# Optimization experiments

Measured on AMD Instinct MI355X. Metric: run time of the kernel, lower is better.

The kernel has to match this reference:

```python
import jax, jax.numpy as jnp
import numpy as np

N_LEVELS = 128.0  # int8: [-128, 127]

def fake_quant(x):
    """Per-tensor int8 fixed-point fake quant (power-of-two scale), STE rounding."""
    maxabs = jnp.max(jnp.abs(x))
    # power-of-two scale covering maxabs, as in Brevitas *FixedPoint quantizers
    scale = jnp.exp2(jnp.ceil(jnp.log2(jnp.maximum(maxabs, 1e-10)))) / N_LEVELS
    scale = jax.lax.stop_gradient(scale)
    xs = x / scale
    q = jnp.clip(jnp.round(xs), -N_LEVELS, N_LEVELS - 1.0)
    q = xs + jax.lax.stop_gradient(q - xs)  # straight-through estimator
    return q * scale


def setup_inputs() -> dict:
    key = jax.random.key(0)
    k1, k2, k3, k4 = jax.random.split(key, 4)
    B, T, D, H = 512, 2048, 10, 20
    x = jax.random.normal(k1, (B, T, D), dtype=jnp.float32)
    h0 = jnp.zeros((B, H), dtype=jnp.float32)
    W_ih = jax.random.normal(k2, (H, D), dtype=jnp.float32) * 0.3
    W_hh = jax.random.normal(k3, (H, H), dtype=jnp.float32) * 0.2
    b = jax.random.normal(k4, (H,), dtype=jnp.float32) * 0.1
    return {"x": x, "h0": h0, "W_ih": W_ih, "W_hh": W_hh, "b": b}


def reference(x, h0, W_ih, W_hh, b):
    # io quant on input and initial state
    xq = fake_quant(x)
    h = fake_quant(h0)
    # weight / bias quant (per-tensor fixed point)
    Wi = fake_quant(W_ih)
    Wh = fake_quant(W_hh)
    bq = fake_quant(b)
    # precompute input-hidden contribution for all timesteps: [B,T,H]
    xW = jnp.einsum('btd,hd->bth', xq, Wi) + bq

    def step(h_prev, xw_t):
        acc = xw_t + h_prev @ Wh.T          # gate accumulation [B,H]
        acc = fake_quant(acc)               # gate_acc_quant
        h_new = jnp.tanh(acc)               # vanilla RNN nonlinearity
        out = fake_quant(h_new)             # io_quant on output/hidden
        return out, out

    xW_t = jnp.swapaxes(xW, 0, 1)           # [T,B,H]
    _, outs = jax.lax.scan(step, h, xW_t)   # outs: [T,B,H]
    return jnp.swapaxes(outs, 0, 1)         # batch_first output [B,T,H]
```

## Files before the change

kernel.cpp:

```cpp
#include <hip/hip_runtime.h>
#include <math.h>

#define BB 512
#define TT 2048
#define DD 10
#define HH 20
#define BH (BB*HH)

#define WS_AMAX     0
#define WS_PROD_XWI 4
#define WS_INV_SX   5
#define WS_S_H0     6
#define WS_INV_SH0  7
#define WS_S_WH     8
#define WS_BQ       16
#define WS_WIP      40
#define WS_WHP      104
#define WS_XW_OFF   4096

#define BAR() asm volatile("s_waitcnt lgkmcnt(0)\n\ts_barrier" ::: "memory")

__device__ __forceinline__ int dot4(int a, int b, int c) {
#if defined(__has_builtin)
#if __has_builtin(__builtin_amdgcn_sdot4)
    return __builtin_amdgcn_sdot4(a, b, c, false);
#define DOT4_DONE 1
#endif
#endif
#ifndef DOT4_DONE
    int r = c;
    r += ((a << 24) >> 24) * ((b << 24) >> 24);
    r += ((a << 16) >> 24) * ((b << 16) >> 24);
    r += ((a << 8) >> 24) * ((b << 8) >> 24);
    r += (a >> 24) * (b >> 24);
    return r;
#endif
}

__device__ __forceinline__ void p2s(float m, float* s, float* is) {
    m = fmaxf(m, 1e-10f);
    unsigned u = __float_as_uint(m);
    int k = (int)(u >> 23) - 127 + ((u & 0x7fffffu) ? 1 : 0);
    *s  = __uint_as_float((unsigned)(k + 120) << 23);
    *is = __uint_as_float((unsigned)(134 - k) << 23);
}

__device__ __forceinline__ int qlevel(float v, float inv) {
    return (int)fminf(fmaxf(rintf(v * inv), -128.f), 127.f);
}

__device__ __forceinline__ int pack4(int a, int b, int c, int d) {
    return (a & 255) | ((b & 255) << 8) | ((c & 255) << 16) | ((d & 255) << 24);
}

__global__ void k_amax(const float* __restrict__ x, int n4, unsigned* amax) {
    int g = blockIdx.x * blockDim.x + threadIdx.x;
    int stride = gridDim.x * blockDim.x;
    const float4* xv = (const float4*)x;
    float m = 0.f;
    for (int i = g; i < n4; i += stride) {
        float4 v = xv[i];
        m = fmaxf(m, fmaxf(fmaxf(fabsf(v.x), fabsf(v.y)), fmaxf(fabsf(v.z), fabsf(v.w))));
    }
#pragma unroll
    for (int off = 32; off; off >>= 1) m = fmaxf(m, __shfl_xor(m, off, 64));
    if ((threadIdx.x & 63) == 0) atomicMax(amax, __float_as_uint(m));
}

__device__ float bmaxabs(const float* p, int n, float* red, int tid) {
    float m = 0.f;
    for (int i = tid; i < n; i += 256) m = fmaxf(m, fabsf(p[i]));
    red[tid] = m; __syncthreads();
    for (int s = 128; s; s >>= 1) {
        if (tid < s) red[tid] = fmaxf(red[tid], red[tid + s]);
        __syncthreads();
    }
    m = red[0]; __syncthreads();
    return m;
}

__global__ void k_prep(const float* __restrict__ Wi, const float* __restrict__ Wh,
                       const float* __restrict__ bias, const float* __restrict__ h0,
                       float* wsf, int* wsi) {
    __shared__ float red[256];
    __shared__ float hdr[4];
    int tid = threadIdx.x;
    float mwi = bmaxabs(Wi, HH * DD, red, tid);
    float mwh = bmaxabs(Wh, HH * HH, red, tid);
    float mb  = bmaxabs(bias, HH, red, tid);
    float mh0 = bmaxabs(h0, BH, red, tid);
    if (tid == 0) {
        float mx = __uint_as_float(((unsigned*)wsf)[WS_AMAX]);
        float sx, isx, swi, iswi, swh, iswh, sb, isb, sh0, ish0;
        p2s(mx,  &sx,  &isx);
        p2s(mwi, &swi, &iswi);
        p2s(mwh, &swh, &iswh);
        p2s(mb,  &sb,  &isb);
        p2s(mh0, &sh0, &ish0);
        wsf[WS_PROD_XWI] = sx * swi;
        wsf[WS_INV_SX]   = isx;
        wsf[WS_S_H0]     = sh0;
        wsf[WS_INV_SH0]  = ish0;
        wsf[WS_S_WH]     = swh;
        hdr[0] = iswi; hdr[1] = iswh; hdr[2] = sb; hdr[3] = isb;
    }
    __syncthreads();
    if (tid < HH) {
        float iswi = hdr[0], iswh = hdr[1], sb = hdr[2], isb = hdr[3];
        int lv[20];
#pragma unroll
        for (int d = 0; d < DD; ++d) lv[d] = qlevel(Wi[tid * DD + d], iswi);
        lv[10] = 0; lv[11] = 0;
#pragma unroll
        for (int k = 0; k < 3; ++k)
            wsi[WS_WIP + tid * 3 + k] = pack4(lv[4*k], lv[4*k+1], lv[4*k+2], lv[4*k+3]);
#pragma unroll
        for (int k = 0; k < HH; ++k) lv[k] = qlevel(Wh[tid * HH + k], iswh);
#pragma unroll
        for (int k = 0; k < 5; ++k)
            wsi[WS_WHP + tid * 5 + k] = pack4(lv[4*k], lv[4*k+1], lv[4*k+2], lv[4*k+3]);
        wsf[WS_BQ + tid] = (float)qlevel(bias[tid], isb) * sb;
    }
}

__global__ __launch_bounds__(256) void k_xw(const float* __restrict__ x,
                                            const float* __restrict__ wsf,
                                            const int* __restrict__ wsi,
                                            float* __restrict__ xw) {
    int g = blockIdx.x * 256 + threadIdx.x;
    int b = g & (BB - 1);
    int t = g >> 9;
    float isx  = wsf[WS_INV_SX];
    float prod = wsf[WS_PROD_XWI];
    const float2* xp = (const float2*)(x + ((size_t)b * TT + t) * DD);
    float xv[10];
#pragma unroll
    for (int k = 0; k < 5; ++k) { float2 v = xp[k]; xv[2*k] = v.x; xv[2*k+1] = v.y; }
    int lv[12];
#pragma unroll
    for (int d = 0; d < DD; ++d) lv[d] = qlevel(xv[d], isx);
    lv[10] = 0; lv[11] = 0;
    int xpk[3];
#pragma unroll
    for (int k = 0; k < 3; ++k) xpk[k] = pack4(lv[4*k], lv[4*k+1], lv[4*k+2], lv[4*k+3]);
    float res[20];
#pragma unroll
    for (int j = 0; j < HH; ++j) {
        int ai = 0;
#pragma unroll
        for (int k = 0; k < 3; ++k) ai = dot4(xpk[k], wsi[WS_WIP + j * 3 + k], ai);
        res[j] = (float)ai * prod + wsf[WS_BQ + j];
    }
    float4* op = (float4*)(xw + (size_t)t * BH + b * HH);
#pragma unroll
    for (int k = 0; k < 5; ++k)
        op[k] = make_float4(res[4*k], res[4*k+1], res[4*k+2], res[4*k+3]);
}

__global__ __launch_bounds__(1024) void k_rnn(const float* __restrict__ h0,
                                              const float* __restrict__ wsf,
                                              const int* __restrict__ wsi,
                                              float* __restrict__ xw) {
    __shared__ float2 wred[16];
    __shared__ float4 bc;
    __shared__ int lut[256];
    const int tid = threadIdx.x;
    const int b = tid >> 1;
    const int jb = (tid & 1) * 10;
    const bool isLo = (tid & 1) == 0;
    const float s_wh = wsf[WS_S_WH];
    float sprod = wsf[WS_S_H0] * s_wh;

    int whp[50];
#pragma unroll
    for (int jj = 0; jj < 10; ++jj)
#pragma unroll
        for (int k = 0; k < 5; ++k)
            whp[jj * 5 + k] = wsi[WS_WHP + (jb + jj) * 5 + k];

    int hd[5];
    {
        float ish0 = wsf[WS_INV_SH0];
        const float2* hp = (const float2*)(h0 + b * HH + jb);
        int lv[10];
#pragma unroll
        for (int k = 0; k < 5; ++k) {
            float2 v = hp[k];
            lv[2*k]   = qlevel(v.x, ish0);
            lv[2*k+1] = qlevel(v.y, ish0);
        }
        int PA = pack4(lv[0], lv[1], lv[2], lv[3]);
        int PB = pack4(lv[4], lv[5], lv[6], lv[7]);
        int PC = (lv[8] & 255) | ((lv[9] & 255) << 8);
        int QA = __shfl_xor(PA, 1, 64);
        int QB = __shfl_xor(PB, 1, 64);
        int QC = __shfl_xor(PC, 1, 64);
        int XA = isLo ? PA : QA, XB = isLo ? PB : QB, XC = isLo ? PC : QC;
        int YA = isLo ? QA : PA, YB = isLo ? QB : PB, YC = isLo ? QC : PC;
        hd[0] = XA; hd[1] = XB;
        hd[2] = (XC & 0xFFFF) | (YA << 16);
        hd[3] = ((unsigned)YA >> 16) | (YB << 16);
        hd[4] = ((unsigned)YB >> 16) | (YC << 16);
    }
    float xwA[10];
    {
        const float2* p = (const float2*)(xw + b * HH + jb);
#pragma unroll
        for (int k = 0; k < 5; ++k) { float2 v = p[k]; xwA[2*k] = v.x; xwA[2*k+1] = v.y; }
    }

    for (int t = 0; t < TT; ++t) {
        float xwB[10];
        if (t + 1 < TT) {
            const float2* p = (const float2*)(xw + (size_t)(t + 1) * BH + b * HH + jb);
#pragma unroll
            for (int k = 0; k < 5; ++k) { float2 v = p[k]; xwB[2*k] = v.x; xwB[2*k+1] = v.y; }
        }
        float acc[10];
#pragma unroll
        for (int jj = 0; jj < 10; ++jj) {
            int ai = 0;
#pragma unroll
            for (int k = 0; k < 5; ++k) ai = dot4(hd[k], whp[jj * 5 + k], ai);
            acc[jj] = xwA[jj] + (float)ai * sprod;
        }
        float mx = acc[0], nmi = -acc[0];
#pragma unroll
        for (int jj = 1; jj < 10; ++jj) { mx = fmaxf(mx, acc[jj]); nmi = fmaxf(nmi, -acc[jj]); }
#pragma unroll
        for (int off = 32; off; off >>= 1) {
            mx  = fmaxf(mx,  __shfl_xor(mx,  off, 64));
            nmi = fmaxf(nmi, __shfl_xor(nmi, off, 64));
        }
        if ((tid & 63) == 0) wred[tid >> 6] = make_float2(mx, nmi);
        BAR();
        float isa, sh;
        float sprodN;
        if (tid < 256) {
            float2 p = wred[tid & 15];
            float ma = p.x, nm = p.y;
#pragma unroll
            for (int off = 8; off; off >>= 1) {
                ma = fmaxf(ma, __shfl_xor(ma, off, 64));
                nm = fmaxf(nm, __shfl_xor(nm, off, 64));
            }
            float sa;
            p2s(fmaxf(ma, nm), &sa, &isa);
            float lp = fminf(fmaxf(rintf(ma * isa), -128.f), 127.f);
            float ln = fminf(fmaxf(rintf(-nm * isa), -128.f), 127.f);
            float mlvl = fmaxf(fabsf(lp), fabsf(ln));
            float mh = tanhf(mlvl * sa);
            float ish;
            p2s(mh, &sh, &ish);
            sprodN = sh * s_wh;
            float tq = tanhf((float)(tid - 128) * sa);
            lut[tid] = (int)fminf(fmaxf(rintf(tq * ish), -128.f), 127.f);
            if (tid == 0) bc = make_float4(isa, sh, sprodN, 0.f);
        }
        BAR();
        if (tid >= 256) {
            float4 v = bc;
            isa = v.x; sh = v.y; sprod = v.z;
        } else {
            sprod = sprodN;
        }
        int ql[10];
#pragma unroll
        for (int jj = 0; jj < 10; ++jj) {
            int qi = (int)fminf(fmaxf(rintf(acc[jj] * isa), -128.f), 127.f);
            ql[jj] = lut[128 + qi];
        }
        {
            float2* op = (float2*)(xw + (size_t)t * BH + b * HH + jb);
#pragma unroll
            for (int k = 0; k < 5; ++k)
                op[k] = make_float2((float)ql[2*k] * sh, (float)ql[2*k+1] * sh);
        }
        {
            int PA = pack4(ql[0], ql[1], ql[2], ql[3]);
            int PB = pack4(ql[4], ql[5], ql[6], ql[7]);
            int PC = (ql[8] & 255) | ((ql[9] & 255) << 8);
            int QA = __shfl_xor(PA, 1, 64);
            int QB = __shfl_xor(PB, 1, 64);
            int QC = __shfl_xor(PC, 1, 64);
            int XA = isLo ? PA : QA, XB = isLo ? PB : QB, XC = isLo ? PC : QC;
            int YA = isLo ? QA : PA, YB = isLo ? QB : PB, YC = isLo ? QC : PC;
            hd[0] = XA; hd[1] = XB;
            hd[2] = (XC & 0xFFFF) | (YA << 16);
            hd[3] = ((unsigned)YA >> 16) | (YB << 16);
            hd[4] = ((unsigned)YB >> 16) | (YC << 16);
        }
#pragma unroll
        for (int jj = 0; jj < 10; ++jj) xwA[jj] = xwB[jj];
    }
}

__global__ __launch_bounds__(256) void k_tr(const float* __restrict__ src, float* __restrict__ out) {
    __shared__ float tile[16 * 16 * HH];
    int t0 = blockIdx.x * 16, b0 = blockIdx.y * 16;
    for (int i = threadIdx.x; i < 16 * 16 * HH; i += 256) {
        int r = i / (16 * HH), c = i % (16 * HH);
        tile[i] = src[(size_t)(t0 + r) * BH + b0 * HH + c];
    }
    __syncthreads();
    for (int i = threadIdx.x; i < 16 * 16 * HH; i += 256) {
        int bb = i / (16 * HH), rj = i % (16 * HH);
        int r = rj / HH, j = rj % HH;
        out[(size_t)(b0 + bb) * (TT * HH) + (t0 + r) * HH + j] = tile[r * (16 * HH) + bb * HH + j];
    }
}

extern "C" void kernel_launch(void* const* d_in, const int* in_sizes, int n_in,
                              void* d_out, int out_size, void* d_ws, size_t ws_size,
                              hipStream_t stream) {
    const float* x    = (const float*)d_in[0];
    const float* h0   = (const float*)d_in[1];
    const float* Wi   = (const float*)d_in[2];
    const float* Wh   = (const float*)d_in[3];
    const float* bias = (const float*)d_in[4];
    float* out = (float*)d_out;

    char* w = (char*)d_ws;
    float* wsf = (float*)w;
    int* wsi = (int*)w;
    unsigned* amax = (unsigned*)w;
    float* xw = (float*)(w + WS_XW_OFF);

    hipMemsetAsync(d_ws, 0, 64, stream);
    int n = in_sizes[0];
    k_amax<<<2048, 256, 0, stream>>>(x, n / 4, amax);
    k_prep<<<1, 256, 0, stream>>>(Wi, Wh, bias, h0, wsf, wsi);
    k_xw<<<(BB * TT) / 256, 256, 0, stream>>>(x, wsf, wsi, xw);
    k_rnn<<<1, 1024, 0, stream>>>(h0, wsf, wsi, xw);
    k_tr<<<dim3(TT / 16, BB / 16), 256, 0, stream>>>(xw, out);
}
```

Baseline: 5.369 ms.

## Use DPP reductions and redundant per-thread scale computation in RNN step

Replaces the shuffle-based wave max reductions with DPP row/broadcast operations on order-preserving unsigned encodings of the floats. Every thread now recomputes the step's scale factors from the shared per-wave maxima, which drops the broadcast variable and the post-barrier read of it. It also uses fmed3 for clamping, fma for accumulation, DPP quad-permute for the pair exchange, and incremented pointers for addressing. The cost is redundant transcendental work (tanh, p2s) on all 1024 threads each step, in exchange for less latency on the serial critical path.

New measurement: 5.535 ms. +3.1%, slower.

```diff
diff --git a/kernel.cpp b/kernel.cpp
--- a/kernel.cpp
+++ b/kernel.cpp
@@ -21,20 +21,7 @@
 #define BAR() asm volatile("s_waitcnt lgkmcnt(0)\n\ts_barrier" ::: "memory")
 
 __device__ __forceinline__ int dot4(int a, int b, int c) {
-#if defined(__has_builtin)
-#if __has_builtin(__builtin_amdgcn_sdot4)
     return __builtin_amdgcn_sdot4(a, b, c, false);
-#define DOT4_DONE 1
-#endif
-#endif
-#ifndef DOT4_DONE
-    int r = c;
-    r += ((a << 24) >> 24) * ((b << 24) >> 24);
-    r += ((a << 16) >> 24) * ((b << 16) >> 24);
-    r += ((a << 8) >> 24) * ((b << 8) >> 24);
-    r += (a >> 24) * (b >> 24);
-    return r;
-#endif
 }
 
 __device__ __forceinline__ void p2s(float m, float* s, float* is) {
@@ -45,12 +32,57 @@
     *is = __uint_as_float((unsigned)(134 - k) << 23);
 }
 
+__device__ __forceinline__ float fmed3(float a, float b, float c) {
+    return __builtin_amdgcn_fmed3f(a, b, c);
+}
+
 __device__ __forceinline__ int qlevel(float v, float inv) {
-    return (int)fminf(fmaxf(rintf(v * inv), -128.f), 127.f);
+    return (int)fmed3(rintf(v * inv), -128.f, 127.f);
 }
 
 __device__ __forceinline__ int pack4(int a, int b, int c, int d) {
     return (a & 255) | ((b & 255) << 8) | ((c & 255) << 16) | ((d & 255) << 24);
+}
+
+__device__ __forceinline__ unsigned fenc(float x) {
+    unsigned u = __float_as_uint(x);
+    return u ^ (unsigned)(((int)u >> 31) | 0x80000000);
+}
+__device__ __forceinline__ float fdec(unsigned e) {
+    unsigned mask = (~(unsigned)((int)e >> 31)) | 0x80000000u;
+    return __uint_as_float(e ^ mask);
+}
+
+__device__ __forceinline__ unsigned wave_umax(unsigned m) {
+    unsigned t;
+    t = (unsigned)__builtin_amdgcn_update_dpp(0, (int)m, 0x111, 0xf, 0xf, true); m = m > t ? m : t;
+    t = (unsigned)__builtin_amdgcn_update_dpp(0, (int)m, 0x112, 0xf, 0xf, true); m = m > t ? m : t;
+    t = (unsigned)__builtin_amdgcn_update_dpp(0, (int)m, 0x114, 0xf, 0xf, true); m = m > t ? m : t;
+    t = (unsigned)__builtin_amdgcn_update_dpp(0, (int)m, 0x118, 0xf, 0xf, true); m = m > t ? m : t;
+    t = (unsigned)__builtin_amdgcn_update_dpp(0, (int)m, 0x142, 0xa, 0xf, true); m = m > t ? m : t;
+    t = (unsigned)__builtin_amdgcn_update_dpp(0, (int)m, 0x143, 0xc, 0xf, true); m = m > t ? m : t;
+    return m;
+}
+
+__device__ __forceinline__ unsigned row_umax(unsigned m) {
+    unsigned t;
+    t = (unsigned)__builtin_amdgcn_update_dpp(0, (int)m, 0x121, 0xf, 0xf, true); m = m > t ? m : t;
+    t = (unsigned)__builtin_amdgcn_update_dpp(0, (int)m, 0x122, 0xf, 0xf, true); m = m > t ? m : t;
+    t = (unsigned)__builtin_amdgcn_update_dpp(0, (int)m, 0x124, 0xf, 0xf, true); m = m > t ? m : t;
+    t = (unsigned)__builtin_amdgcn_update_dpp(0, (int)m, 0x128, 0xf, 0xf, true); m = m > t ? m : t;
+    return m;
+}
+
+__device__ __forceinline__ void mk_hd(int PA, int PB, int PC, bool isLo, int* hd) {
+    int QA = __builtin_amdgcn_update_dpp(0, PA, 0xB1, 0xf, 0xf, true);
+    int QB = __builtin_amdgcn_update_dpp(0, PB, 0xB1, 0xf, 0xf, true);
+    int QC = __builtin_amdgcn_update_dpp(0, PC, 0xB1, 0xf, 0xf, true);
+    int XA = isLo ? PA : QA, XB = isLo ? PB : QB, XC = isLo ? PC : QC;
+    int YA = isLo ? QA : PA, YB = isLo ? QB : PB, YC = isLo ? QC : PC;
+    hd[0] = XA; hd[1] = XB;
+    hd[2] = (XC & 0xFFFF) | (YA << 16);
+    hd[3] = (int)((unsigned)YA >> 16) | (YB << 16);
+    hd[4] = (int)((unsigned)YB >> 16) | (YC << 16);
 }
 
 __global__ void k_amax(const float* __restrict__ x, int n4, unsigned* amax) {
@@ -161,8 +193,7 @@
                                               const float* __restrict__ wsf,
                                               const int* __restrict__ wsi,
                                               float* __restrict__ xw) {
-    __shared__ float2 wred[16];
-    __shared__ float4 bc;
+    __shared__ uint2 wred[16];
     __shared__ int lut[256];
     const int tid = threadIdx.x;
     const int b = tid >> 1;
@@ -189,18 +220,9 @@
             lv[2*k]   = qlevel(v.x, ish0);
             lv[2*k+1] = qlevel(v.y, ish0);
         }
-        int PA = pack4(lv[0], lv[1], lv[2], lv[3]);
-        int PB = pack4(lv[4], lv[5], lv[6], lv[7]);
-        int PC = (lv[8] & 255) | ((lv[9] & 255) << 8);
-        int QA = __shfl_xor(PA, 1, 64);
-        int QB = __shfl_xor(PB, 1, 64);
-        int QC = __shfl_xor(PC, 1, 64);
-        int XA = isLo ? PA : QA, XB = isLo ? PB : QB, XC = isLo ? PC : QC;
-        int YA = isLo ? QA : PA, YB = isLo ? QB : PB, YC = isLo ? QC : PC;
-        hd[0] = XA; hd[1] = XB;
-        hd[2] = (XC & 0xFFFF) | (YA << 16);
-        hd[3] = ((unsigned)YA >> 16) | (YB << 16);
-        hd[4] = ((unsigned)YB >> 16) | (YC << 16);
+        mk_hd(pack4(lv[0], lv[1], lv[2], lv[3]),
+              pack4(lv[4], lv[5], lv[6], lv[7]),
+              (lv[8] & 255) | ((lv[9] & 255) << 8), isLo, hd);
     }
     float xwA[10];
     {
@@ -208,13 +230,14 @@
 #pragma unroll
         for (int k = 0; k < 5; ++k) { float2 v = p[k]; xwA[2*k] = v.x; xwA[2*k+1] = v.y; }
     }
+    const float2* pf = (const float2*)(xw + (size_t)BH + b * HH + jb);
+    float2*       po = (float2*)(xw + b * HH + jb);
 
     for (int t = 0; t < TT; ++t) {
         float xwB[10];
         if (t + 1 < TT) {
-            const float2* p = (const float2*)(xw + (size_t)(t + 1) * BH + b * HH + jb);
-#pragma unroll
-            for (int k = 0; k < 5; ++k) { float2 v = p[k]; xwB[2*k] = v.x; xwB[2*k+1] = v.y; }
+#pragma unroll
+            for (int k = 0; k < 5; ++k) { float2 v = pf[k]; xwB[2*k] = v.x; xwB[2*k+1] = v.y; }
         }
         float acc[10];
 #pragma unroll
@@ -222,76 +245,46 @@
             int ai = 0;
 #pragma unroll
             for (int k = 0; k < 5; ++k) ai = dot4(hd[k], whp[jj * 5 + k], ai);
-            acc[jj] = xwA[jj] + (float)ai * sprod;
-        }
-        float mx = acc[0], nmi = -acc[0];
-#pragma unroll
-        for (int jj = 1; jj < 10; ++jj) { mx = fmaxf(mx, acc[jj]); nmi = fmaxf(nmi, -acc[jj]); }
-#pragma unroll
-        for (int off = 32; off; off >>= 1) {
-            mx  = fmaxf(mx,  __shfl_xor(mx,  off, 64));
-            nmi = fmaxf(nmi, __shfl_xor(nmi, off, 64));
-        }
-        if ((tid & 63) == 0) wred[tid >> 6] = make_float2(mx, nmi);
+            acc[jj] = fmaf((float)ai, sprod, xwA[jj]);
+        }
+        float mx = acc[0], mn = acc[0];
+#pragma unroll
+        for (int jj = 1; jj < 10; ++jj) { mx = fmaxf(mx, acc[jj]); mn = fminf(mn, acc[jj]); }
+        unsigned ea = wave_umax(fenc(mx));
+        unsigned eb = wave_umax(fenc(-mn));
+        if ((tid & 63) == 63) wred[tid >> 6] = make_uint2(ea, eb);
         BAR();
-        float isa, sh;
-        float sprodN;
+        uint2 wp = wred[tid & 15];
+        float ma = fdec(row_umax(wp.x));
+        float nm = fdec(row_umax(wp.y));
+        float sa, isa; p2s(fmaxf(ma, nm), &sa, &isa);
+        float lp = fmed3(rintf(ma * isa), -128.f, 127.f);
+        float ln = fmed3(rintf(-nm * isa), -128.f, 127.f);
+        float mlvl = fmaxf(fabsf(lp), fabsf(ln));
+        float mh = tanhf(mlvl * sa);
+        float sh, ish; p2s(mh, &sh, &ish);
+        sprod = sh * s_wh;
         if (tid < 256) {
-            float2 p = wred[tid & 15];
-            float ma = p.x, nm = p.y;
-#pragma unroll
-            for (int off = 8; off; off >>= 1) {
-                ma = fmaxf(ma, __shfl_xor(ma, off, 64));
-                nm = fmaxf(nm, __shfl_xor(nm, off, 64));
-            }
-            float sa;
-            p2s(fmaxf(ma, nm), &sa, &isa);
-            float lp = fminf(fmaxf(rintf(ma * isa), -128.f), 127.f);
-            float ln = fminf(fmaxf(rintf(-nm * isa), -128.f), 127.f);
-            float mlvl = fmaxf(fabsf(lp), fabsf(ln));
-            float mh = tanhf(mlvl * sa);
-            float ish;
-            p2s(mh, &sh, &ish);
-            sprodN = sh * s_wh;
             float tq = tanhf((float)(tid - 128) * sa);
-            lut[tid] = (int)fminf(fmaxf(rintf(tq * ish), -128.f), 127.f);
-            if (tid == 0) bc = make_float4(isa, sh, sprodN, 0.f);
+            lut[tid] = (int)fmed3(rintf(tq * ish), -128.f, 127.f);
         }
         BAR();
-        if (tid >= 256) {
-            float4 v = bc;
-            isa = v.x; sh = v.y; sprod = v.z;
-        } else {
-            sprod = sprodN;
-        }
         int ql[10];
 #pragma unroll
         for (int jj = 0; jj < 10; ++jj) {
-            int qi = (int)fminf(fmaxf(rintf(acc[jj] * isa), -128.f), 127.f);
-            ql[jj] = lut[128 + qi];
-        }
-        {
-            float2* op = (float2*)(xw + (size_t)t * BH + b * HH + jb);
-#pragma unroll
-            for (int k = 0; k < 5; ++k)
-                op[k] = make_float2((float)ql[2*k] * sh, (float)ql[2*k+1] * sh);
-        }
-        {
-            int PA = pack4(ql[0], ql[1], ql[2], ql[3]);
-            int PB = pack4(ql[4], ql[5], ql[6], ql[7]);
-            int PC = (ql[8] & 255) | ((ql[9] & 255) << 8);
-            int QA = __shfl_xor(PA, 1, 64);
-            int QB = __shfl_xor(PB, 1, 64);
-            int QC = __shfl_xor(PC, 1, 64);
-            int XA = isLo ? PA : QA, XB = isLo ? PB : QB, XC = isLo ? PC : QC;
-            int YA = isLo ? QA : PA, YB = isLo ? QB : PB, YC = isLo ? QC : PC;
-            hd[0] = XA; hd[1] = XB;
-            hd[2] = (XC & 0xFFFF) | (YA << 16);
-            hd[3] = ((unsigned)YA >> 16) | (YB << 16);
-            hd[4] = ((unsigned)YB >> 16) | (YC << 16);
-        }
+            int qi = (int)fmed3(rintf(acc[jj] * isa), -128.f, 127.f);
+            ql[jj] = lut[qi + 128];
+        }
+#pragma unroll
+        for (int k = 0; k < 5; ++k)
+            po[k] = make_float2((float)ql[2*k] * sh, (float)ql[2*k+1] * sh);
+        mk_hd(pack4(ql[0], ql[1], ql[2], ql[3]),
+              pack4(ql[4], ql[5], ql[6], ql[7]),
+              (ql[8] & 255) | ((ql[9] & 255) << 8), isLo, hd);
 #pragma unroll
         for (int jj = 0; jj < 10; ++jj) xwA[jj] = xwB[jj];
+        pf += BH / 2;
+        po += BH / 2;
     }
 }
 
```
